# Kernel tuning notes

Measured on AMD Instinct MI355X. Metric: run time of the kernel, lower is better.

## Reference

```python
import jax, jax.numpy as jnp
import numpy as np

B, S, H = 32, 1024, 1024

def setup_inputs() -> dict:
    key = jax.random.key(0)
    k1, k2, k3, k4, k5 = jax.random.split(key, 5)
    scale = 1.0 / np.sqrt(H)
    return {
        "decoder_hidden": jax.random.normal(k1, (B, H), jnp.float32),
        "encoder_outputs": jax.random.normal(k2, (B, S, H), jnp.float32),
        "U_w": jax.random.normal(k3, (H, H), jnp.float32) * scale,
        "W_w": jax.random.normal(k4, (H, H), jnp.float32) * scale,
        "v_w": jax.random.normal(k5, (H,), jnp.float32) * scale,
    }

def reference(decoder_hidden, encoder_outputs, U_w, W_w, v_w):
    # U(decoder_hidden): [B, H] @ [H, H]^T -> [B, H], broadcast over S
    U_h = jnp.einsum('bh,oh->bo', decoder_hidden, U_w)          # [B, H]
    W_s = jnp.einsum('bsh,oh->bso', encoder_outputs, W_w)       # [B, S, H]
    # v(tanh(U_h + W_s)) -> attention scores [B, S]
    att = jnp.einsum('bsh,h->bs', jnp.tanh(U_h[:, None, :] + W_s), v_w)
    alpha = jax.nn.softmax(att, axis=1)                          # [B, S]
    context = jnp.einsum('bs,bsh->bh', alpha, encoder_outputs)   # [B, H]
    return (context, alpha)
```

## Files before the change

kernel.cpp:

```cpp
#include <hip/hip_runtime.h>
#include <hip/hip_bf16.h>
#include <cstdint>
#include <cstddef>

#define B_DIM 32
#define S_DIM 1024
#define H_DIM 1024
#define M_DIM (B_DIM * S_DIM)

typedef __attribute__((ext_vector_type(8))) short bf16x8;
typedef __attribute__((ext_vector_type(4))) float f32x4;

static __device__ __forceinline__ unsigned short f2bf(float f) {
  unsigned u = __float_as_uint(f);
  u = (u + 0x7FFFu + ((u >> 16) & 1u)) >> 16;
  return (unsigned short)u;
}
static __device__ __forceinline__ float bf2f(unsigned short u) {
  return __uint_as_float(((unsigned)u) << 16);
}
static __device__ __forceinline__ float fast_tanh(float x) {
  return 1.f - 2.f / (__expf(2.f * x) + 1.f);
}

static __device__ __forceinline__ void gload16(const unsigned short* g, char* l) {
  __builtin_amdgcn_global_load_lds(
      (const __attribute__((address_space(1))) unsigned int*)g,
      (__attribute__((address_space(3))) unsigned int*)l, 16, 0, 0);
}

__global__ void k_prep_all(const float* __restrict__ E, unsigned short* __restrict__ Eb,
                           const float* __restrict__ W, unsigned short* __restrict__ Wb,
                           const float* __restrict__ dh, const float* __restrict__ Uw,
                           float* __restrict__ Uh) {
  const int bid = blockIdx.x;
  if (bid < 1024) {
    const int wave = threadIdx.x >> 6;
    const int lane = threadIdx.x & 63;
    const int o = bid;
    float uw[16];
#pragma unroll
    for (int k = 0; k < 16; ++k) uw[k] = Uw[o * H_DIM + k * 64 + lane];
#pragma unroll
    for (int bb = 0; bb < 8; ++bb) {
      const int b = wave * 8 + bb;
      float acc = 0.f;
#pragma unroll
      for (int k = 0; k < 16; ++k) acc += uw[k] * dh[b * H_DIM + k * 64 + lane];
#pragma unroll
      for (int msk = 32; msk >= 1; msk >>= 1) acc += __shfl_xor(acc, msk, 64);
      if (lane == 0) Uh[b * H_DIM + o] = acc;
    }
  } else if (bid < 2048) {
    const int idx = (bid - 1024) * 256 + threadIdx.x;
    float4 v = ((const float4*)W)[idx];
    ushort4 o;
    o.x = f2bf(v.x); o.y = f2bf(v.y); o.z = f2bf(v.z); o.w = f2bf(v.w);
    ((ushort4*)Wb)[idx] = o;
  } else {
    const int n8 = M_DIM * (H_DIM / 8);
    const int stride = 2048 * 256;
    for (int idx = (bid - 2048) * 256 + threadIdx.x; idx < n8; idx += stride) {
      const float4* gp = (const float4*)(E + (size_t)idx * 8);
      float4 lo = gp[0], hi = gp[1];
      bf16x8 w;
      w[0] = (short)f2bf(lo.x); w[1] = (short)f2bf(lo.y);
      w[2] = (short)f2bf(lo.z); w[3] = (short)f2bf(lo.w);
      w[4] = (short)f2bf(hi.x); w[5] = (short)f2bf(hi.y);
      w[6] = (short)f2bf(hi.z); w[7] = (short)f2bf(hi.w);
      *(bf16x8*)(Eb + (size_t)idx * 8) = w;
    }
  }
}

#define A5_BM 256
#define A5_BN 256
#define A5_BUF 65536
#define NT_FAST 4

__launch_bounds__(512, 2)
__global__ void k_att6(const unsigned short* __restrict__ Eb,
                       const unsigned short* __restrict__ Wb,
                       const float* __restrict__ Uh,
                       const float* __restrict__ vw,
                       float* __restrict__ att_p) {
  __shared__ __align__(16) char lds[2 * A5_BUF];

  const int bid = blockIdx.x;
  const int xj = bid & 7;
  const int q  = bid >> 3;
  const int n_tile = q & 3;
  const int m_tile = ((q >> 2) << 3) | xj;
  const int m0 = m_tile * A5_BM;
  const int n0 = n_tile * A5_BN;
  const int b  = m0 >> 10;

  const int tid  = threadIdx.x;
  const int wid  = tid >> 6;
  const int lane = tid & 63;
  const int wm = (wid >> 2) * 128;
  const int wn = (wid & 3) * 64;

  size_t offA[4], offB[4];
  int ldsA[4], ldsB[4];
#pragma unroll
  for (int j = 0; j < 4; ++j) {
    const int chunk = j * 512 + tid;
    const int r  = chunk >> 3;
    const int c8 = (chunk & 7) ^ (r & 7);
    offA[j] = (size_t)(m0 + r) * H_DIM + c8 * 8;
    offB[j] = (size_t)(n0 + r) * H_DIM + c8 * 8;
    ldsA[j] = j * 8192 + wid * 1024;
    ldsB[j] = 32768 + j * 8192 + wid * 1024;
  }

  auto stage = [&](int t) {
    char* dst = lds + (t & 1) * A5_BUF;
    const size_t k0 = (size_t)t * 64;
#pragma unroll
    for (int j = 0; j < 4; ++j) gload16(Eb + offA[j] + k0, dst + ldsA[j]);
#pragma unroll
    for (int j = 0; j < 4; ++j) gload16(Wb + offB[j] + k0, dst + ldsB[j]);
  };

  const int fr_row = lane & 15;
  const int fr_k8  = lane >> 4;

  f32x4 acc[8][4];
#pragma unroll
  for (int mf = 0; mf < 8; ++mf)
#pragma unroll
    for (int nf = 0; nf < 4; ++nf) acc[mf][nf] = (f32x4)(0.0f);

  stage(0);

  for (int t = 0; t < 16; ++t) {
    asm volatile("s_waitcnt vmcnt(0)" ::: "memory");
    __builtin_amdgcn_s_barrier();
    asm volatile("" ::: "memory");

    if (t < 15) stage(t + 1);

    const char* As = lds + (t & 1) * A5_BUF;
    const char* Bs = As + 32768;

#pragma unroll
    for (int kh = 0; kh < 2; ++kh) {
      const int kb = kh * 32 + fr_k8 * 8;
      bf16x8 af[8], bfr[4];
#pragma unroll
      for (int mf = 0; mf < 8; ++mf) {
        const int row = wm + mf * 16 + fr_row;
        const int addr = (row * 128 + kb * 2) ^ ((row & 7) << 4);
        af[mf] = *(const bf16x8*)(As + addr);
      }
#pragma unroll
      for (int nf = 0; nf < 4; ++nf) {
        const int row = wn + nf * 16 + fr_row;
        const int addr = (row * 128 + kb * 2) ^ ((row & 7) << 4);
        bfr[nf] = *(const bf16x8*)(Bs + addr);
      }
      __builtin_amdgcn_s_setprio(1);
#pragma unroll
      for (int mf = 0; mf < 8; ++mf)
#pragma unroll
        for (int nf = 0; nf < 4; ++nf)
          acc[mf][nf] = __builtin_amdgcn_mfma_f32_16x16x32_bf16(af[mf], bfr[nf], acc[mf][nf], 0, 0, 0);
      __builtin_amdgcn_s_setprio(0);
    }
  }

  float* red = (float*)lds;

  const int col = lane & 15;
  const int rhi = lane >> 4;
  float uh[4], vv[4];
#pragma unroll
  for (int nf = 0; nf < 4; ++nf) {
    const int o = n0 + wn + nf * 16 + col;
    uh[nf] = Uh[b * H_DIM + o];
    vv[nf] = vw[o];
  }
#pragma unroll
  for (int mf = 0; mf < 8; ++mf) {
    float rs[4];
#pragma unroll
    for (int jj = 0; jj < 4; ++jj) {
      float s = 0.f;
#pragma unroll
      for (int nf = 0; nf < 4; ++nf) {
        const float x = acc[mf][nf][jj] + uh[nf];
        s += fast_tanh(x) * vv[nf];
      }
      rs[jj] = s;
    }
#pragma unroll
    for (int msk = 1; msk < 16; msk <<= 1) {
#pragma unroll
      for (int jj = 0; jj < 4; ++jj) rs[jj] += __shfl_xor(rs[jj], msk, 64);
    }
    if (col == 0) {
#pragma unroll
      for (int jj = 0; jj < 4; ++jj) {
        const int local = mf * 16 + rhi * 4 + jj;
        red[wid * 128 + local] = rs[jj];
      }
    }
  }
  __syncthreads();
  if (tid < 256) {
    const int mhalf = tid >> 7;
    const int loc = tid & 127;
    float sum = 0.f;
#pragma unroll
    for (int j = 0; j < 4; ++j) sum += red[(mhalf * 4 + j) * 128 + loc];
    att_p[(size_t)n_tile * M_DIM + m0 + tid] = sum;
  }
}

__global__ void k_ctx_sm(const unsigned short* __restrict__ Eb,
                         const float* __restrict__ att_p,
                         float* __restrict__ alpha_out,
                         float* __restrict__ ctx_p) {
  const int bid = blockIdx.x;
  const int b  = bid >> 2;
  const int sq = bid & 3;
  const int tid = threadIdx.x;
  __shared__ float red[8];
  __shared__ float qa[256];

  float a[4];
  float mx = -1e30f;
#pragma unroll
  for (int i = 0; i < 4; ++i) {
    const int s = i * 256 + tid;
    float v = 0.f;
#pragma unroll
    for (int t = 0; t < NT_FAST; ++t) v += att_p[(size_t)t * M_DIM + b * S_DIM + s];
    a[i] = v;
    mx = fmaxf(mx, v);
  }
#pragma unroll
  for (int msk = 32; msk >= 1; msk >>= 1) mx = fmaxf(mx, __shfl_xor(mx, msk, 64));
  if ((tid & 63) == 0) red[tid >> 6] = mx;
  __syncthreads();
  mx = fmaxf(fmaxf(red[0], red[1]), fmaxf(red[2], red[3]));
  float sum = 0.f;
#pragma unroll
  for (int i = 0; i < 4; ++i) { a[i] = __expf(a[i] - mx); sum += a[i]; }
#pragma unroll
  for (int msk = 32; msk >= 1; msk >>= 1) sum += __shfl_xor(sum, msk, 64);
  if ((tid & 63) == 0) red[4 + (tid >> 6)] = sum;
  __syncthreads();
  const float inv = 1.f / (red[4] + red[5] + red[6] + red[7]);
  if (sq == 0) {
#pragma unroll
    for (int i = 0; i < 4; ++i) alpha_out[b * S_DIM + i * 256 + tid] = a[i] * inv;
  }
  qa[tid] = a[sq] * inv;
  __syncthreads();

  const int h = tid * 4;
  const unsigned short* ep = Eb + (size_t)b * S_DIM * H_DIM + (size_t)(sq * 256) * H_DIM + h;
  float4 acc = make_float4(0.f, 0.f, 0.f, 0.f);
  for (int s = 0; s < 256; ++s) {
    const float al = qa[s];
    ushort4 v = *(const ushort4*)(ep + (size_t)s * H_DIM);
    acc.x += al * bf2f(v.x);
    acc.y += al * bf2f(v.y);
    acc.z += al * bf2f(v.z);
    acc.w += al * bf2f(v.w);
  }
  *(float4*)&ctx_p[(size_t)sq * (B_DIM * H_DIM) + b * H_DIM + h] = acc;
}

__global__ void k_ctx_reduce(const float* __restrict__ ctx_p, float* __restrict__ ctx) {
  const int i = blockIdx.x * 256 + threadIdx.x;
  ctx[i] = ctx_p[i] + ctx_p[32768 + i] + ctx_p[65536 + i] + ctx_p[98304 + i];
}

extern "C" void kernel_launch(void* const* d_in, const int* in_sizes, int n_in,
                              void* d_out, int out_size, void* d_ws, size_t ws_size,
                              hipStream_t stream) {
  (void)in_sizes; (void)n_in; (void)out_size; (void)ws_size;
  const float* dh  = (const float*)d_in[0];
  const float* enc = (const float*)d_in[1];
  const float* Uw  = (const float*)d_in[2];
  const float* Ww  = (const float*)d_in[3];
  const float* vw  = (const float*)d_in[4];
  float* ctx_out = (float*)d_out;
  float* alpha   = (float*)d_out + M_DIM;

  char* ws = (char*)d_ws;
  const size_t EB_BYTES = (size_t)M_DIM * H_DIM * 2;

  unsigned short* Eb = (unsigned short*)ws;
  unsigned short* Wb = (unsigned short*)(ws + EB_BYTES);
  float* Uh    = (float*)(ws + EB_BYTES + (2u << 20));
  float* att_p = (float*)(ws + EB_BYTES + (2u << 20) + (128u << 10));
  float* ctx_p = (float*)(ws + EB_BYTES + (2u << 20) + (128u << 10) + (1u << 20));

  k_prep_all<<<4096, 256, 0, stream>>>(enc, Eb, Ww, Wb, dh, Uw, Uh);
  k_att6<<<512, 512, 0, stream>>>(Eb, Wb, Uh, vw, att_p);
  k_ctx_sm<<<128, 256, 0, stream>>>(Eb, att_p, alpha, ctx_p);
  k_ctx_reduce<<<128, 256, 0, stream>>>(ctx_p, ctx_out);
}
```

Before: 129.1 us.

## Load W operand fragments directly from global memory instead of staging through LDS

The GEMM kernel no longer stages the W (B-operand) tile into shared memory. Each wave now loads its B fragments straight from global memory into registers at the start of every k-step, and LDS shrinks to hold only the A tile, half the previous footprint. This cuts LDS traffic and footprint, and may allow more blocks per CU. In exchange, the global B loads are issued right after the barrier with little latency hiding, and B data is re-read by the waves that share the same columns, relying on the L2 cache.

After: 168.3 us. 1.3x slower.

```diff
diff --git a/kernel.cpp b/kernel.cpp
--- a/kernel.cpp
+++ b/kernel.cpp
@@ -75,16 +75,16 @@
 
 #define A5_BM 256
 #define A5_BN 256
-#define A5_BUF 65536
+#define A10_BUF 32768
 #define NT_FAST 4
 
 __launch_bounds__(512, 2)
-__global__ void k_att6(const unsigned short* __restrict__ Eb,
-                       const unsigned short* __restrict__ Wb,
-                       const float* __restrict__ Uh,
-                       const float* __restrict__ vw,
-                       float* __restrict__ att_p) {
-  __shared__ __align__(16) char lds[2 * A5_BUF];
+__global__ void k_att10(const unsigned short* __restrict__ Eb,
+                        const unsigned short* __restrict__ Wb,
+                        const float* __restrict__ Uh,
+                        const float* __restrict__ vw,
+                        float* __restrict__ att_p) {
+  __shared__ __align__(16) char lds[2 * A10_BUF];
 
   const int bid = blockIdx.x;
   const int xj = bid & 7;
@@ -101,30 +101,31 @@
   const int wm = (wid >> 2) * 128;
   const int wn = (wid & 3) * 64;
 
-  size_t offA[4], offB[4];
-  int ldsA[4], ldsB[4];
+  size_t offA[4];
+  int ldsA[4];
 #pragma unroll
   for (int j = 0; j < 4; ++j) {
     const int chunk = j * 512 + tid;
     const int r  = chunk >> 3;
     const int c8 = (chunk & 7) ^ (r & 7);
     offA[j] = (size_t)(m0 + r) * H_DIM + c8 * 8;
-    offB[j] = (size_t)(n0 + r) * H_DIM + c8 * 8;
     ldsA[j] = j * 8192 + wid * 1024;
-    ldsB[j] = 32768 + j * 8192 + wid * 1024;
   }
 
   auto stage = [&](int t) {
-    char* dst = lds + (t & 1) * A5_BUF;
+    char* dst = lds + (t & 1) * A10_BUF;
     const size_t k0 = (size_t)t * 64;
 #pragma unroll
     for (int j = 0; j < 4; ++j) gload16(Eb + offA[j] + k0, dst + ldsA[j]);
-#pragma unroll
-    for (int j = 0; j < 4; ++j) gload16(Wb + offB[j] + k0, dst + ldsB[j]);
   };
 
   const int fr_row = lane & 15;
   const int fr_k8  = lane >> 4;
+
+  const unsigned short* bp[4];
+#pragma unroll
+  for (int nf = 0; nf < 4; ++nf)
+    bp[nf] = Wb + (size_t)(n0 + wn + nf * 16 + fr_row) * H_DIM + fr_k8 * 8;
 
   f32x4 acc[8][4];
 #pragma unroll
@@ -139,33 +140,34 @@
     __builtin_amdgcn_s_barrier();
     asm volatile("" ::: "memory");
 
+    bf16x8 bfr[4][2];
+#pragma unroll
+    for (int nf = 0; nf < 4; ++nf)
+#pragma unroll
+      for (int kh = 0; kh < 2; ++kh)
+        bfr[nf][kh] = *(const bf16x8*)(bp[nf] + (size_t)t * 64 + kh * 32);
+    __builtin_amdgcn_sched_barrier(0);
+
     if (t < 15) stage(t + 1);
 
-    const char* As = lds + (t & 1) * A5_BUF;
-    const char* Bs = As + 32768;
+    const char* As = lds + (t & 1) * A10_BUF;
 
 #pragma unroll
     for (int kh = 0; kh < 2; ++kh) {
       const int kb = kh * 32 + fr_k8 * 8;
-      bf16x8 af[8], bfr[4];
+      bf16x8 af[8];
 #pragma unroll
       for (int mf = 0; mf < 8; ++mf) {
         const int row = wm + mf * 16 + fr_row;
         const int addr = (row * 128 + kb * 2) ^ ((row & 7) << 4);
         af[mf] = *(const bf16x8*)(As + addr);
       }
-#pragma unroll
-      for (int nf = 0; nf < 4; ++nf) {
-        const int row = wn + nf * 16 + fr_row;
-        const int addr = (row * 128 + kb * 2) ^ ((row & 7) << 4);
-        bfr[nf] = *(const bf16x8*)(Bs + addr);
-      }
       __builtin_amdgcn_s_setprio(1);
 #pragma unroll
       for (int mf = 0; mf < 8; ++mf)
 #pragma unroll
         for (int nf = 0; nf < 4; ++nf)
-          acc[mf][nf] = __builtin_amdgcn_mfma_f32_16x16x32_bf16(af[mf], bfr[nf], acc[mf][nf], 0, 0, 0);
+          acc[mf][nf] = __builtin_amdgcn_mfma_f32_16x16x32_bf16(af[mf], bfr[nf][kh], acc[mf][nf], 0, 0, 0);
       __builtin_amdgcn_s_setprio(0);
     }
   }
@@ -301,7 +303,7 @@
   float* ctx_p = (float*)(ws + EB_BYTES + (2u << 20) + (128u << 10) + (1u << 20));
 
   k_prep_all<<<4096, 256, 0, stream>>>(enc, Eb, Ww, Wb, dh, Uw, Uh);
-  k_att6<<<512, 512, 0, stream>>>(Eb, Wb, Uh, vw, att_p);
+  k_att10<<<512, 512, 0, stream>>>(Eb, Wb, Uh, vw, att_p);
   k_ctx_sm<<<128, 256, 0, stream>>>(Eb, att_p, alpha, ctx_p);
   k_ctx_reduce<<<128, 256, 0, stream>>>(ctx_p, ctx_out);
 }
```
